# Kernel tuning notes

Hardware: AMD Instinct MI355X
Metric: run time of the kernel (lower is better)

## Reference

```python
import jax, jax.numpy as jnp
import numpy as np

B, N, D, E, A, DIAM = 16, 1024, 128, 16384, 64, 3


def setup_inputs() -> dict:
    key = jax.random.key(0)
    ks = jax.random.split(key, 20)
    s = 0.05
    inp = {
        "node_features": jax.random.normal(ks[0], (B, N, D), jnp.float32),
        "edge_features": jax.random.normal(ks[1], (B, N, N), jnp.float32),
        "src_idx": jax.random.randint(ks[2], (E,), 0, N, jnp.int32),
        "tgt_idx": jax.random.randint(ks[3], (E,), 0, N, jnp.int32),
        # message MLP: Linear(2D+1 -> D)
        "W_msg": jax.random.normal(ks[4], (2 * D + 1, D), jnp.float32) * s,
        "b_msg": jax.random.normal(ks[5], (D,), jnp.float32) * s,
        # GRUCell(D, D), gate order r,z,n (torch convention)
        "W_ih": jax.random.normal(ks[6], (3 * D, D), jnp.float32) * s,
        "W_hh": jax.random.normal(ks[7], (3 * D, D), jnp.float32) * s,
        "b_ih": jax.random.normal(ks[8], (3 * D,), jnp.float32) * s,
        "b_hh": jax.random.normal(ks[9], (3 * D,), jnp.float32) * s,
        # readout: Linear(D,D)+SELU, Linear(D,D)+SELU, then policy head Linear(D,A)
        "W_r1": jax.random.normal(ks[10], (D, D), jnp.float32) * s,
        "b_r1": jax.random.normal(ks[11], (D,), jnp.float32) * s,
        "W_r2": jax.random.normal(ks[12], (D, D), jnp.float32) * s,
        "b_r2": jax.random.normal(ks[13], (D,), jnp.float32) * s,
        "W_pol": jax.random.normal(ks[14], (D, A), jnp.float32) * s,
        "b_pol": jax.random.normal(ks[15], (A,), jnp.float32) * s,
    }
    return inp


def reference(node_features, edge_features, src_idx, tgt_idx,
              W_msg, b_msg, W_ih, W_hh, b_ih, b_hh,
              W_r1, b_r1, W_r2, b_r2, W_pol, b_pol):
    h = node_features  # [B, N, D]
    ef = edge_features[:, src_idx, tgt_idx][..., None]  # [B, E, 1], constant across rounds
    for _ in range(DIAM):
        src_f = h[:, src_idx]  # [B, E, D] gather
        tgt_f = h[:, tgt_idx]  # [B, E, D]
        comb = jnp.concatenate([src_f, tgt_f, ef], axis=-1)  # [B, E, 2D+1]
        msg = jax.nn.selu(comb @ W_msg + b_msg)  # [B, E, D]
        # scatter-sum messages onto target nodes
        agg = jax.vmap(lambda m: jax.ops.segment_sum(m, tgt_idx, num_segments=N))(msg)  # [B, N, D]
        # GRUCell update (torch math, gate order r,z,n; b_hn stays inside r*(...))
        gi = agg @ W_ih.T + b_ih  # [B, N, 3D]
        gh = h @ W_hh.T + b_hh    # [B, N, 3D]
        i_r, i_z, i_n = jnp.split(gi, 3, axis=-1)
        h_r, h_z, h_n = jnp.split(gh, 3, axis=-1)
        r = jax.nn.sigmoid(i_r + h_r)
        z = jax.nn.sigmoid(i_z + h_z)
        n = jnp.tanh(i_n + r * h_n)
        h = (1.0 - z) * n + z * h
    pooled = h.sum(axis=1)  # [B, D]
    pooled = jax.nn.selu(pooled @ W_r1 + b_r1)
    pooled = jax.nn.selu(pooled @ W_r2 + b_r2)
    return pooled @ W_pol + b_pol  # [B, A] policy logits
```

## Files before the change

### kernel.cpp

```cpp
#include <hip/hip_runtime.h>
#include <hip/hip_bf16.h>
#include <math.h>

constexpr int kB = 16;
constexpr int kN = 1024;
constexpr int kD = 128;
constexpr int kE = 16384;

typedef short bf16x8 __attribute__((ext_vector_type(8)));
typedef float f32x4 __attribute__((ext_vector_type(4)));
typedef unsigned short us4 __attribute__((ext_vector_type(4)));

__device__ __forceinline__ float selu_f(float x) {
    const float scale = 1.0507009873554805f;
    const float alpha = 1.6732632423543772f;
    return x > 0.f ? scale * x : scale * alpha * (expf(x) - 1.f);
}

__device__ __forceinline__ float sigmoid_f(float x) {
    return 1.f / (1.f + expf(-x));
}

__device__ __forceinline__ float bf2f(unsigned short u) {
    union { unsigned int i; float f; } x;
    x.i = ((unsigned int)u) << 16;
    return x.f;
}

__device__ __forceinline__ unsigned short f2bf(float f) {
    union { float f; unsigned int i; } u;
    u.f = f;
    const unsigned int r = u.i + 0x7fffu + ((u.i >> 16) & 1u);
    return (unsigned short)(r >> 16);
}

__global__ void k_count(const int* __restrict__ tgt, int* __restrict__ cnt) {
    int e = blockIdx.x * 256 + threadIdx.x;
    atomicAdd(&cnt[tgt[e]], 1);
}

__global__ void k_scan(const int* __restrict__ cnt, int* __restrict__ cursor,
                       int* __restrict__ rowstart) {
    __shared__ int s[kN];
    int t = threadIdx.x;
    int own = cnt[t];
    s[t] = own;
    __syncthreads();
    for (int off = 1; off < kN; off <<= 1) {
        int add = (t >= off) ? s[t - off] : 0;
        __syncthreads();
        s[t] += add;
        __syncthreads();
    }
    int excl = s[t] - own;
    cursor[t] = excl;
    rowstart[t] = excl;
    if (t == kN - 1) rowstart[kN] = s[t];
}

__global__ void k_scatter(const int* __restrict__ src, const int* __restrict__ tgt,
                          int* __restrict__ cursor, int* __restrict__ sid,
                          int* __restrict__ ssrc) {
    int e = blockIdx.x * 256 + threadIdx.x;
    int tg = tgt[e];
    int pos = atomicAdd(&cursor[tg], 1);
    sid[pos] = e;
    ssrc[pos] = src[e];
}

__global__ void k_gather_ef(const float* __restrict__ edgef, const int* __restrict__ src,
                            const int* __restrict__ tgt, const int* __restrict__ sid,
                            float* __restrict__ efg) {
    int gid = blockIdx.x * 256 + threadIdx.x;
    int b = gid >> 14;
    int i = gid & (kE - 1);
    int eid = sid[i];
    efg[gid] = edgef[(size_t)b * kN * kN + (size_t)src[eid] * kN + tgt[eid]];
}

__global__ void k_h0(const float* __restrict__ nodef, float* __restrict__ h,
                     unsigned short* __restrict__ h_bf) {
    int gid = blockIdx.x * 256 + threadIdx.x;
    float v = nodef[gid];
    h[gid] = v;
    h_bf[gid] = f2bf(v);
}

__global__ void k_buildw(const float* __restrict__ Wmsg, const float* __restrict__ Whh,
                         const float* __restrict__ Wih,
                         const float* __restrict__ bih, const float* __restrict__ bhh,
                         unsigned short* __restrict__ WcatT,
                         unsigned short* __restrict__ Wfused,
                         float* __restrict__ bihP, float* __restrict__ bhhP) {
    const int j = blockIdx.x;
    const int k = threadIdx.x;
    if (j < 256) {
        float v = (j < 128) ? Wmsg[k * 128 + j] : Wmsg[(128 + k) * 128 + (j - 128)];
        WcatT[j * 128 + k] = f2bf(v);
    } else {
        const int f = j - 256;
        const int dg = f / 48, rem = f % 48;
        const int g = rem / 16, di = rem % 16;
        const int orig = g * 128 + dg * 16 + di;
        Wfused[(size_t)f * 256 + k] = f2bf(Wih[(size_t)orig * 128 + k]);
        Wfused[(size_t)f * 256 + 128 + k] = f2bf(Whh[(size_t)orig * 128 + k]);
        if (k == 0) {
            bihP[f] = bih[orig];
            bhhP[f] = bhh[orig];
        }
    }
}

__launch_bounds__(256)
__global__ void k_mm256(const unsigned short* __restrict__ A,
                        const unsigned short* __restrict__ Bt,
                        unsigned short* __restrict__ HST) {
    __shared__ uint4 As[2048];
    __shared__ uint4 Bs[2048];
    const int t = threadIdx.x;
    const int r0 = blockIdx.x * 128;
    const int c0 = blockIdx.y * 128;
    const uint4* gA = (const uint4*)(A + (size_t)r0 * 128);
    const uint4* gB = (const uint4*)(Bt + (size_t)c0 * 128);
#pragma unroll
    for (int i = 0; i < 8; ++i) {
        const int f = i * 256 + t;
        const int row = f >> 4, c16 = f & 15;
        const int d = row * 16 + (c16 ^ (row & 7));
        As[d] = gA[f];
        Bs[d] = gB[f];
    }
    __syncthreads();
    const int w = t >> 6, l = t & 63;
    const int wm = (w & 1) * 64, wn = (w >> 1) * 64;
    const int lin = l & 15, kq = l >> 4;
    f32x4 acc[4][4] = {};
#pragma unroll
    for (int s = 0; s < 4; ++s) {
        bf16x8 a[4], b[4];
#pragma unroll
        for (int mi = 0; mi < 4; ++mi) {
            const int row = wm + mi * 16 + lin;
            a[mi] = *(const bf16x8*)&As[row * 16 + ((s * 4 + kq) ^ (row & 7))];
        }
#pragma unroll
        for (int ni = 0; ni < 4; ++ni) {
            const int row = wn + ni * 16 + lin;
            b[ni] = *(const bf16x8*)&Bs[row * 16 + ((s * 4 + kq) ^ (row & 7))];
        }
#pragma unroll
        for (int mi = 0; mi < 4; ++mi)
#pragma unroll
            for (int ni = 0; ni < 4; ++ni)
                acc[mi][ni] = __builtin_amdgcn_mfma_f32_16x16x32_bf16(
                    a[mi], b[ni], acc[mi][ni], 0, 0, 0);
    }
    const int rq = kq * 4;
#pragma unroll
    for (int ni = 0; ni < 4; ++ni) {
        const int col = c0 + wn + ni * 16 + lin;
#pragma unroll
        for (int mi = 0; mi < 4; ++mi) {
            const int row = r0 + wm + mi * 16 + rq;
#pragma unroll
            for (int r = 0; r < 4; ++r)
                HST[(size_t)(row + r) * 256 + col] = f2bf(acc[mi][ni][r]);
        }
    }
}

__launch_bounds__(256)
__global__ void k_edge(const unsigned short* __restrict__ HST, const float* __restrict__ efg,
                       const int* __restrict__ ssrc, const int* __restrict__ rowstart,
                       const float* __restrict__ Wmsg, const float* __restrict__ bmsg,
                       unsigned short* __restrict__ agg_bf) {
    __shared__ float4 part[2][4][32];
    const int t = threadIdx.x;
    const int b = blockIdx.y;
    const int tl = t >> 7;
    const int tg = blockIdx.x * 2 + tl;
    const int slot = (t >> 5) & 3;
    const int lane = t & 31;
    const int c = lane * 4;
    const float4 w3 = *(const float4*)&Wmsg[256 * 128 + c];
    const float4 bm = *(const float4*)&bmsg[c];
    const size_t base = (size_t)b * kN;
    const us4 htu = *(const us4*)&HST[(base + tg) * 256 + 128 + c];
    const float hb0 = bf2f(htu.x) + bm.x;
    const float hb1 = bf2f(htu.y) + bm.y;
    const float hb2 = bf2f(htu.z) + bm.z;
    const float hb3 = bf2f(htu.w) + bm.w;
    const float* efb = efg + b * kE;
    const int j0 = rowstart[tg], j1 = rowstart[tg + 1];
    float a0 = 0.f, a1 = 0.f, a2 = 0.f, a3 = 0.f;
    for (int j = j0 + slot; j < j1; j += 4) {
        const int s = ssrc[j];
        const float ef = efb[j];
        const us4 hs = *(const us4*)&HST[(base + s) * 256 + c];
        a0 += selu_f(bf2f(hs.x) + fmaf(ef, w3.x, hb0));
        a1 += selu_f(bf2f(hs.y) + fmaf(ef, w3.y, hb1));
        a2 += selu_f(bf2f(hs.z) + fmaf(ef, w3.z, hb2));
        a3 += selu_f(bf2f(hs.w) + fmaf(ef, w3.w, hb3));
    }
    part[tl][slot][lane] = make_float4(a0, a1, a2, a3);
    __syncthreads();
    if (slot == 0) {
        const float4 p1 = part[tl][1][lane];
        const float4 p2 = part[tl][2][lane];
        const float4 p3 = part[tl][3][lane];
        a0 += p1.x + p2.x + p3.x;
        a1 += p1.y + p2.y + p3.y;
        a2 += p1.z + p2.z + p3.z;
        a3 += p1.w + p2.w + p3.w;
        us4 o;
        o.x = f2bf(a0);
        o.y = f2bf(a1);
        o.z = f2bf(a2);
        o.w = f2bf(a3);
        *(us4*)&agg_bf[(base + tg) * 128 + c] = o;
    }
}

__launch_bounds__(256)
__global__ void k_gigru(const unsigned short* __restrict__ agg_bf,
                        const unsigned short* __restrict__ h_bf_in,
                        const unsigned short* __restrict__ Wfused,
                        const float* __restrict__ bihP, const float* __restrict__ bhhP,
                        float* __restrict__ h, unsigned short* __restrict__ h_bf_out,
                        float* __restrict__ pooled, int lastIter) {
    __shared__ uint4 As[2048];
    __shared__ uint4 Bs[1536];
    const int t = threadIdx.x;
    const int r0 = blockIdx.x * 128;
    const int y = blockIdx.y;
    const int w = t >> 6, l = t & 63;
    const int wm = (w & 1) * 64, wc0 = (w >> 1) * 48;
    const int lin = l & 15, kq = l >> 4, rq = kq * 4;
    f32x4 acc[4][3] = {};
    f32x4 accN[4] = {};
#pragma unroll
    for (int stage = 0; stage < 2; ++stage) {
        const unsigned short* Ap = stage ? h_bf_in : agg_bf;
        const uint4* gA = (const uint4*)(Ap + (size_t)r0 * 128);
#pragma unroll
        for (int i = 0; i < 8; ++i) {
            const int f = i * 256 + t;
            const int row = f >> 4, c16 = f & 15;
            As[row * 16 + (c16 ^ (row & 7))] = gA[f];
        }
        const uint4* gW = (const uint4*)Wfused;
#pragma unroll
        for (int i = 0; i < 6; ++i) {
            const int f = i * 256 + t;
            const int j = f >> 4, c16 = f & 15;
            Bs[j * 16 + (c16 ^ (j & 7))] = gW[(size_t)(y * 96 + j) * 32 + stage * 16 + c16];
        }
        __syncthreads();
#pragma unroll
        for (int ks = 0; ks < 4; ++ks) {
            bf16x8 a[4], b[3];
#pragma unroll
            for (int mi = 0; mi < 4; ++mi) {
                const int row = wm + mi * 16 + lin;
                a[mi] = *(const bf16x8*)&As[row * 16 + ((ks * 4 + kq) ^ (row & 7))];
            }
#pragma unroll
            for (int ni = 0; ni < 3; ++ni) {
                const int row = wc0 + ni * 16 + lin;
                b[ni] = *(const bf16x8*)&Bs[row * 16 + ((ks * 4 + kq) ^ (row & 7))];
            }
#pragma unroll
            for (int mi = 0; mi < 4; ++mi) {
                acc[mi][0] = __builtin_amdgcn_mfma_f32_16x16x32_bf16(a[mi], b[0], acc[mi][0], 0, 0, 0);
                acc[mi][1] = __builtin_amdgcn_mfma_f32_16x16x32_bf16(a[mi], b[1], acc[mi][1], 0, 0, 0);
                if (stage == 0)
                    acc[mi][2] = __builtin_amdgcn_mfma_f32_16x16x32_bf16(a[mi], b[2], acc[mi][2], 0, 0, 0);
                else
                    accN[mi] = __builtin_amdgcn_mfma_f32_16x16x32_bf16(a[mi], b[2], accN[mi], 0, 0, 0);
            }
        }
        __syncthreads();
    }
    const int colR = y * 96 + wc0 + lin;
    const float bR = bihP[colR] + bhhP[colR];
    const float bZ = bihP[colR + 16] + bhhP[colR + 16];
    const float biN = bihP[colR + 32];
    const float bhN = bhhP[colR + 32];
    const int dgg = y * 2 + (wc0 / 48);
    const int d = dgg * 16 + lin;
    const int bb = r0 >> 10;
    float psum = 0.f;
#pragma unroll
    for (int mi = 0; mi < 4; ++mi) {
#pragma unroll
        for (int r = 0; r < 4; ++r) {
            const int row = r0 + wm + mi * 16 + rq + r;
            const float rr = sigmoid_f(acc[mi][0][r] + bR);
            const float zz = sigmoid_f(acc[mi][1][r] + bZ);
            const float i_n = acc[mi][2][r] + biN;
            const float h_n = accN[mi][r] + bhN;
            const float nn = tanhf(fmaf(rr, h_n, i_n));
            const size_t idx = (size_t)row * 128 + d;
            const float hv = h[idx];
            const float o = fmaf(zz, hv - nn, nn);
            h[idx] = o;
            h_bf_out[idx] = f2bf(o);
            psum += o;
        }
    }
    if (lastIter) atomicAdd(&pooled[bb * 128 + d], psum);
}

__global__ void k_head(const float* __restrict__ pooled,
                       const float* __restrict__ Wr1, const float* __restrict__ br1,
                       const float* __restrict__ Wr2, const float* __restrict__ br2,
                       const float* __restrict__ Wpol, const float* __restrict__ bpol,
                       float* __restrict__ out) {
    __shared__ float p[128], t1[128];
    const int b = blockIdx.x, d = threadIdx.x;
    p[d] = pooled[b * 128 + d];
    __syncthreads();
    float acc = br1[d];
    for (int k = 0; k < 128; ++k) acc = fmaf(p[k], Wr1[k * 128 + d], acc);
    t1[d] = selu_f(acc);
    __syncthreads();
    acc = br2[d];
    for (int k = 0; k < 128; ++k) acc = fmaf(t1[k], Wr2[k * 128 + d], acc);
    __syncthreads();
    p[d] = selu_f(acc);
    __syncthreads();
    if (d < 64) {
        float o = bpol[d];
        for (int k = 0; k < 128; ++k) o = fmaf(p[k], Wpol[k * 64 + d], o);
        out[b * 64 + d] = o;
    }
}

extern "C" void kernel_launch(void* const* d_in, const int* in_sizes, int n_in,
                              void* d_out, int out_size, void* d_ws, size_t ws_size,
                              hipStream_t stream) {
    const float* nodef = (const float*)d_in[0];
    const float* edgef = (const float*)d_in[1];
    const int* src = (const int*)d_in[2];
    const int* tgt = (const int*)d_in[3];
    const float* Wmsg = (const float*)d_in[4];
    const float* bmsg = (const float*)d_in[5];
    const float* Wih = (const float*)d_in[6];
    const float* Whh = (const float*)d_in[7];
    const float* bih = (const float*)d_in[8];
    const float* bhh = (const float*)d_in[9];
    const float* Wr1 = (const float*)d_in[10];
    const float* br1 = (const float*)d_in[11];
    const float* Wr2 = (const float*)d_in[12];
    const float* br2 = (const float*)d_in[13];
    const float* Wpol = (const float*)d_in[14];
    const float* bpol = (const float*)d_in[15];
    float* out = (float*)d_out;

    float* ws = (float*)d_ws;
    float* h = ws;
    float* efg = h + 2097152;
    float* bihP = efg + 262144;
    float* bhhP = bihP + 384;
    float* pooled = bhhP + 384;
    unsigned short* HST = (unsigned short*)(pooled + 2048);
    unsigned short* h_bf = HST + 4194304;
    unsigned short* agg_bf = h_bf + 2097152;
    unsigned short* WcatT = agg_bf + 2097152;
    unsigned short* Wfused = WcatT + 32768;
    int* cnt = (int*)(Wfused + 98304);
    int* cursor = cnt + 1024;
    int* rowstart = cursor + 1024;
    int* sid = rowstart + 1040;
    int* ssrc = sid + 16384;

    hipMemsetAsync(cnt, 0, 1024 * sizeof(int), stream);
    hipMemsetAsync(pooled, 0, 2048 * sizeof(float), stream);
    k_h0<<<(kB * kN * kD) / 256, 256, 0, stream>>>(nodef, h, h_bf);
    k_count<<<kE / 256, 256, 0, stream>>>(tgt, cnt);
    k_scan<<<1, 1024, 0, stream>>>(cnt, cursor, rowstart);
    k_scatter<<<kE / 256, 256, 0, stream>>>(src, tgt, cursor, sid, ssrc);
    k_gather_ef<<<(kB * kE) / 256, 256, 0, stream>>>(edgef, src, tgt, sid, efg);
    k_buildw<<<640, 128, 0, stream>>>(Wmsg, Whh, Wih, bih, bhh, WcatT, Wfused, bihP, bhhP);

    for (int it = 0; it < 3; ++it) {
        k_mm256<<<dim3(128, 2), 256, 0, stream>>>(h_bf, WcatT, HST);
        k_edge<<<dim3(kN / 2, kB), 256, 0, stream>>>(HST, efg, ssrc, rowstart, Wmsg, bmsg, agg_bf);
        k_gigru<<<dim3(128, 4), 256, 0, stream>>>(agg_bf, h_bf, Wfused, bihP, bhhP, h, h_bf,
                                                  pooled, it == 2 ? 1 : 0);
    }

    k_head<<<kB, 128, 0, stream>>>(pooled, Wr1, br1, Wr2, br2, Wpol, bpol, out);
}
```

Before: 312.7 us.

## Drop fp32 hidden state, read h from shared tile, ping-pong bf16 buffers

Removes the fp32 copy of the hidden state. The GRU update now reads the previous h value from the bf16 tile already staged in shared memory during the h@W_hh stage, instead of loading it from global memory. The bf16 hidden state is double-buffered so one kernel's input and output no longer alias. The h0 conversion and edge counting are merged into one kernel, and the two memsets become one. Holding the GRU residual at bf16 precision adds some numerical error across the three rounds.

```diff
diff --git a/kernel.cpp b/kernel.cpp
--- a/kernel.cpp
+++ b/kernel.cpp
@@ -34,9 +34,11 @@
     return (unsigned short)(r >> 16);
 }
 
-__global__ void k_count(const int* __restrict__ tgt, int* __restrict__ cnt) {
-    int e = blockIdx.x * 256 + threadIdx.x;
-    atomicAdd(&cnt[tgt[e]], 1);
+__global__ void k_h0c(const float* __restrict__ nodef, unsigned short* __restrict__ h_bf,
+                      const int* __restrict__ tgt, int* __restrict__ cnt) {
+    int gid = blockIdx.x * 256 + threadIdx.x;
+    h_bf[gid] = f2bf(nodef[gid]);
+    if (gid < kE) atomicAdd(&cnt[tgt[gid]], 1);
 }
 
 __global__ void k_scan(const int* __restrict__ cnt, int* __restrict__ cursor,
@@ -76,14 +78,6 @@
     int i = gid & (kE - 1);
     int eid = sid[i];
     efg[gid] = edgef[(size_t)b * kN * kN + (size_t)src[eid] * kN + tgt[eid]];
-}
-
-__global__ void k_h0(const float* __restrict__ nodef, float* __restrict__ h,
-                     unsigned short* __restrict__ h_bf) {
-    int gid = blockIdx.x * 256 + threadIdx.x;
-    float v = nodef[gid];
-    h[gid] = v;
-    h_bf[gid] = f2bf(v);
 }
 
 __global__ void k_buildw(const float* __restrict__ Wmsg, const float* __restrict__ Whh,
@@ -226,7 +220,7 @@
                         const unsigned short* __restrict__ h_bf_in,
                         const unsigned short* __restrict__ Wfused,
                         const float* __restrict__ bihP, const float* __restrict__ bhhP,
-                        float* __restrict__ h, unsigned short* __restrict__ h_bf_out,
+                        unsigned short* __restrict__ h_bf_out,
                         float* __restrict__ pooled, int lastIter) {
     __shared__ uint4 As[2048];
     __shared__ uint4 Bs[1536];
@@ -289,22 +283,21 @@
     const int dgg = y * 2 + (wc0 / 48);
     const int d = dgg * 16 + lin;
     const int bb = r0 >> 10;
+    const int dc = d >> 3, de = d & 7;
     float psum = 0.f;
 #pragma unroll
     for (int mi = 0; mi < 4; ++mi) {
 #pragma unroll
         for (int r = 0; r < 4; ++r) {
-            const int row = r0 + wm + mi * 16 + rq + r;
+            const int rowL = wm + mi * 16 + rq + r;
             const float rr = sigmoid_f(acc[mi][0][r] + bR);
             const float zz = sigmoid_f(acc[mi][1][r] + bZ);
             const float i_n = acc[mi][2][r] + biN;
             const float h_n = accN[mi][r] + bhN;
             const float nn = tanhf(fmaf(rr, h_n, i_n));
-            const size_t idx = (size_t)row * 128 + d;
-            const float hv = h[idx];
+            const float hv = bf2f(((const unsigned short*)&As[rowL * 16 + (dc ^ (rowL & 7))])[de]);
             const float o = fmaf(zz, hv - nn, nn);
-            h[idx] = o;
-            h_bf_out[idx] = f2bf(o);
+            h_bf_out[(size_t)(r0 + rowL) * 128 + d] = f2bf(o);
             psum += o;
         }
     }
@@ -358,35 +351,35 @@
     float* out = (float*)d_out;
 
     float* ws = (float*)d_ws;
-    float* h = ws;
-    float* efg = h + 2097152;
+    float* efg = ws;
     float* bihP = efg + 262144;
     float* bhhP = bihP + 384;
-    float* pooled = bhhP + 384;
+    int* cnt = (int*)(bhhP + 384);
+    float* pooled = (float*)(cnt + 1024);
     unsigned short* HST = (unsigned short*)(pooled + 2048);
-    unsigned short* h_bf = HST + 4194304;
-    unsigned short* agg_bf = h_bf + 2097152;
+    unsigned short* hbfA = HST + 4194304;
+    unsigned short* hbfB = hbfA + 2097152;
+    unsigned short* agg_bf = hbfB + 2097152;
     unsigned short* WcatT = agg_bf + 2097152;
     unsigned short* Wfused = WcatT + 32768;
-    int* cnt = (int*)(Wfused + 98304);
-    int* cursor = cnt + 1024;
+    int* cursor = (int*)(Wfused + 98304);
     int* rowstart = cursor + 1024;
     int* sid = rowstart + 1040;
     int* ssrc = sid + 16384;
 
-    hipMemsetAsync(cnt, 0, 1024 * sizeof(int), stream);
-    hipMemsetAsync(pooled, 0, 2048 * sizeof(float), stream);
-    k_h0<<<(kB * kN * kD) / 256, 256, 0, stream>>>(nodef, h, h_bf);
-    k_count<<<kE / 256, 256, 0, stream>>>(tgt, cnt);
+    hipMemsetAsync(cnt, 0, (1024 + 2048) * sizeof(int), stream);
+    k_h0c<<<(kB * kN * kD) / 256, 256, 0, stream>>>(nodef, hbfA, tgt, cnt);
     k_scan<<<1, 1024, 0, stream>>>(cnt, cursor, rowstart);
     k_scatter<<<kE / 256, 256, 0, stream>>>(src, tgt, cursor, sid, ssrc);
     k_gather_ef<<<(kB * kE) / 256, 256, 0, stream>>>(edgef, src, tgt, sid, efg);
     k_buildw<<<640, 128, 0, stream>>>(Wmsg, Whh, Wih, bih, bhh, WcatT, Wfused, bihP, bhhP);
 
     for (int it = 0; it < 3; ++it) {
-        k_mm256<<<dim3(128, 2), 256, 0, stream>>>(h_bf, WcatT, HST);
+        unsigned short* hcur = (it & 1) ? hbfB : hbfA;
+        unsigned short* hnxt = (it & 1) ? hbfA : hbfB;
+        k_mm256<<<dim3(128, 2), 256, 0, stream>>>(hcur, WcatT, HST);
         k_edge<<<dim3(kN / 2, kB), 256, 0, stream>>>(HST, efg, ssrc, rowstart, Wmsg, bmsg, agg_bf);
-        k_gigru<<<dim3(128, 4), 256, 0, stream>>>(agg_bf, h_bf, Wfused, bihP, bhhP, h, h_bf,
+        k_gigru<<<dim3(128, 4), 256, 0, stream>>>(agg_bf, hcur, Wfused, bihP, bhhP, hnxt,
                                                   pooled, it == 2 ? 1 : 0);
     }
 
```

Result: faster. 299.5 us (-4.2%).
